# Performance work log

Hardware: AMD Instinct MI355X
Metric: run time of the kernel (lower is better)

## Reference

```python
import jax, jax.numpy as jnp
import numpy as np

BN_EPS = 1e-5
SG = jax.lax.stop_gradient


def _silu(z):
    return z * jax.nn.sigmoid(z)


def _binary_activation(x):
    # forward value = sign(x); backward goes through piecewise quadratic out3 (STE)
    out1 = jnp.where(x < -1, -1.0, x * x + 2 * x)
    out2 = jnp.where(x < 0, out1, -x * x + 2 * x)
    out3 = jnp.where(x < 1, out2, 1.0)
    return SG(jnp.sign(x)) - SG(out3) + out3


def _binarize_weight(w):
    # per-output-channel scaling factor * sign(w), STE through clipped weights
    sf = SG(jnp.mean(jnp.abs(w), axis=(1, 2, 3), keepdims=True))  # [O,1,1,1]
    cw = jnp.clip(w, -1.0, 1.0)
    return SG(sf * jnp.sign(w)) - SG(cw) + cw


def _conv3x3_s2(x, w, b):
    y = jax.lax.conv_general_dilated(
        x, w, window_strides=(2, 2), padding=((1, 1), (1, 1)),
        dimension_numbers=("NCHW", "OIHW", "NCHW"))
    return y + b[None, :, None, None]


def _batchnorm_train(x, gamma, beta):
    # training-mode BN: batch statistics over (N,H,W), biased variance
    mean = jnp.mean(x, axis=(0, 2, 3), keepdims=True)
    var = jnp.mean((x - mean) ** 2, axis=(0, 2, 3), keepdims=True)
    xhat = (x - mean) * jax.lax.rsqrt(var + BN_EPS)
    return xhat * gamma[None, :, None, None] + beta[None, :, None, None]


def _learnable_bias(x, emb, w, b):
    # bias = zero_module(linear)(SiLU(emb)) broadcast over H,W
    bias = _silu(emb) @ w.T + b  # [B, C]
    return x + bias[:, :, None, None]


def _avgpool2(x):
    B, C, H, W = x.shape
    return x.reshape(B, C, H // 2, 2, W // 2, 2).mean(axis=(3, 5))


def setup_inputs() -> dict:
    key = jax.random.key(0)
    ks = jax.random.split(key, 16)
    B, Cin, P, E, H, W = 32, 128, 256, 512, 64, 64
    scalor = P // Cin  # 2
    inp = {
        "x": jax.random.normal(ks[0], (B, Cin, H, W), jnp.float32),
        "emb": jax.random.normal(ks[1], (B, E), jnp.float32),
        "m1_w": jax.random.normal(ks[2], (Cin, E), jnp.float32) * 0.02,
        "m1_b": jnp.zeros((Cin,), jnp.float32),
        "conv_w": jax.random.uniform(ks[3], (scalor, Cin, Cin, 3, 3), jnp.float32, -1.0, 1.0) * 0.1,
        "conv_b": jax.random.normal(ks[4], (scalor, Cin), jnp.float32) * 0.01,
        "bn_g": jnp.ones((scalor, Cin), jnp.float32),
        "bn_b": jnp.zeros((scalor, Cin), jnp.float32),
        "m2_w": jax.random.normal(ks[5], (P, E), jnp.float32) * 0.02,
        "m2_b": jnp.zeros((P,), jnp.float32),
        "prelu_a": jnp.full((P,), 0.25, jnp.float32),
        "m3_w": jax.random.normal(ks[6], (P, E), jnp.float32) * 0.02,
        "m3_b": jnp.zeros((P,), jnp.float32),
    }
    return inp


def reference(x, emb, m1_w, m1_b, conv_w, conv_b, bn_g, bn_b,
              m2_w, m2_b, prelu_a, m3_w, m3_b):
    scalor = conv_w.shape[0]
    out = _learnable_bias(x, emb, m1_w, m1_b)
    out = _binary_activation(out)
    xp = _avgpool2(x)  # residual, [B,Cin,H/2,W/2]
    out_list = []
    for i in range(scalor):
        bw = _binarize_weight(conv_w[i])
        y = _conv3x3_s2(out, bw, conv_b[i])
        y = _batchnorm_train(y, bn_g[i], bn_b[i])
        out_list.append(y + xp)
    o = jnp.concatenate(out_list, axis=1)  # [B, planes, H/2, W/2]
    o = _learnable_bias(o, emb, m2_w, m2_b)
    a = prelu_a[None, :, None, None]
    o = jnp.where(o > 0, o, a * o)  # PReLU per channel
    o = _learnable_bias(o, emb, m3_w, m3_b)
    return o
```

## Files before the change

### kernel.cpp

```cpp
#include <hip/hip_runtime.h>
#include <cstdint>
#include <cstddef>

#define B_  32
#define CIN 128
#define P_  256
#define E_  512
#define H_  64
#define W_  64
#define HO  32
#define WO  32

__global__ void k_bw(const float* __restrict__ emb,
                     const float* __restrict__ m1_w, const float* __restrict__ m1_b,
                     const float* __restrict__ m2_w, const float* __restrict__ m2_b,
                     const float* __restrict__ m3_w, const float* __restrict__ m3_b,
                     const float* __restrict__ conv_w,
                     float* __restrict__ b1, float* __restrict__ b2, float* __restrict__ b3,
                     float* __restrict__ sf, unsigned int* __restrict__ wbits,
                     float* __restrict__ s1, float* __restrict__ s2) {
    int bid = blockIdx.x;
    int tid = threadIdx.x;
    int wave = tid >> 6, lane = tid & 63;

    if (bid < B_ * 160) {
        int n = bid / 160, rg = bid % 160;
        int row = rg * 4 + wave;
        const float* sp = emb + n * E_;
        const float* wrow; float bias; float* dst;
        if (row < CIN)            { wrow = m1_w + (size_t)row * E_;          bias = m1_b[row]; dst = b1 + n * CIN + row; }
        else if (row < CIN + P_)  { int c = row - CIN;      wrow = m2_w + (size_t)c * E_; bias = m2_b[c]; dst = b2 + n * P_ + c; }
        else                      { int c = row - CIN - P_; wrow = m3_w + (size_t)c * E_; bias = m3_b[c]; dst = b3 + n * P_ + c; }
        float acc = 0.f;
        #pragma unroll
        for (int j = 0; j < 8; j++) {
            int k = j * 64 + lane;
            float e = sp[k];
            acc += (e / (1.f + expf(-e))) * wrow[k];
        }
        #pragma unroll
        for (int off = 32; off > 0; off >>= 1) acc += __shfl_down(acc, off);
        if (lane == 0) *dst = acc + bias;
        return;
    }

    int base = (bid - B_ * 160) * 2;
    int oc = base + (wave >> 1);
    int iw = wave & 1;
    int i  = iw * 64 + lane;
    if (lane == 0 && iw == 0) { s1[oc] = 0.f; s2[oc] = 0.f; }
    const float* wp = conv_w + ((size_t)oc * CIN + i) * 9;
    float w[9]; float s = 0.f;
    #pragma unroll
    for (int t = 0; t < 9; t++) { w[t] = wp[t]; s += fabsf(w[t]); }
    #pragma unroll
    for (int t = 0; t < 9; t++) {
        unsigned long long m = __ballot(w[t] < 0.f);
        if (lane == 0) {
            wbits[oc * 36 + t * 4 + iw * 2 + 0] = (unsigned int)(m & 0xffffffffull);
            wbits[oc * 36 + t * 4 + iw * 2 + 1] = (unsigned int)(m >> 32);
        }
    }
    #pragma unroll
    for (int off = 32; off > 0; off >>= 1) s += __shfl_down(s, off);
    __shared__ float sred[4];
    if (lane == 0) sred[wave] = s;
    __syncthreads();
    if (tid == 0)        sf[base]     = (sred[0] + sred[1]) / 1152.f;
    else if (tid == 128) sf[base + 1] = (sred[2] + sred[3]) / 1152.f;
}

__global__ void k_prep(const float* __restrict__ x, const float* __restrict__ b1,
                       unsigned int* __restrict__ abits, float* __restrict__ xpool) {
    __shared__ float sb1[CIN];
    int n = blockIdx.x >> 5, h2 = blockIdx.x & 31;
    int tid = threadIdx.x;
    for (int i = tid; i < CIN; i += 256) sb1[i] = b1[n * CIN + i];
    __syncthreads();

    int pix = tid >> 1, half = tid & 1;
    int h = 2 * h2 + (pix >> 6), w = pix & 63;
    const float* xp = x + ((size_t)n * CIN + half * 64) * (H_ * W_) + (size_t)h * W_ + w;
    unsigned int wds[2];
    #pragma unroll
    for (int wd = 0; wd < 2; wd++) {
        unsigned int m = 0;
        #pragma unroll
        for (int b = 0; b < 32; b++) {
            float v = xp[(size_t)(wd * 32 + b) * (H_ * W_)] + sb1[half * 64 + wd * 32 + b];
            m |= (v < 0.f ? 1u : 0u) << b;
        }
        wds[wd] = m;
    }
    ((uint2*)abits)[((size_t)n * 4096 + (size_t)h * 64 + w) * 2 + half] = make_uint2(wds[0], wds[1]);

    for (int idx = tid; idx < CIN * WO; idx += 256) {
        int c = idx >> 5, w2 = idx & 31;
        const float* p = x + ((size_t)n * CIN + c) * (H_ * W_) + (size_t)(2 * h2) * W_ + 2 * w2;
        float2 a = *(const float2*)p;
        float2 b = *(const float2*)(p + W_);
        xpool[((size_t)n * CIN + c) * (HO * WO) + h2 * WO + w2] = 0.25f * (a.x + a.y + b.x + b.y);
    }
}

__global__ void __launch_bounds__(256, 4) k_conv(const unsigned int* __restrict__ abits,
                                                 const unsigned int* __restrict__ wbits,
                                                 const float* __restrict__ sf,
                                                 float* __restrict__ y) {
    int bid = blockIdx.x;
    int strip = bid & 3, ocg = (bid >> 2) & 7, n = bid >> 5;
    int tid = threadIdx.x;
    int oh = strip * 8 + (tid >> 5), ow = tid & 31;

    const uint4* asrc = ((const uint4*)abits) + ((size_t)n << 12);
    uint4 img[9]; int vmask = 0;
    #pragma unroll
    for (int kh = 0; kh < 3; kh++) {
        #pragma unroll
        for (int kw = 0; kw < 3; kw++) {
            int t = kh * 3 + kw;
            int r = 2 * oh - 1 + kh, c = 2 * ow - 1 + kw;
            bool v = (unsigned)r < 64u && (unsigned)c < 64u;
            img[t] = v ? asrc[r * 64 + c] : make_uint4(0u, 0u, 0u, 0u);
            vmask |= (v ? 1 : 0) << t;
        }
    }
    int base128 = 128 * __popc(vmask);

    const uint4* wp = ((const uint4*)wbits) + (size_t)ocg * 32 * 9;
    const float* sfp = sf + ocg * 32;
    float* yp = y + (((size_t)n * P_ + ocg * 32) << 10) + strip * 256 + tid;
    #pragma unroll 4
    for (int o = 0; o < 32; o++) {
        int popsum = 0;
        #pragma unroll
        for (int t = 0; t < 9; t++) {
            uint4 a = img[t];
            uint4 w = wp[o * 9 + t];
            int p = __popc(a.x ^ w.x) + __popc(a.y ^ w.y) +
                    __popc(a.z ^ w.z) + __popc(a.w ^ w.w);
            popsum += ((vmask >> t) & 1) ? p : 0;
        }
        yp[(size_t)o << 10] = sfp[o] * (float)(base128 - 2 * popsum);
    }
}

__global__ void k_stats(const float* __restrict__ y,
                        float* __restrict__ s1, float* __restrict__ s2) {
    int c = blockIdx.x >> 2, q = blockIdx.x & 3;
    int tid = threadIdx.x;
    float s = 0.f, ss = 0.f;
    for (int n = q * 8; n < q * 8 + 8; n++) {
        float4 v = ((const float4*)y)[(((size_t)n * P_ + c) << 8) + tid];
        s  += v.x + v.y + v.z + v.w;
        ss += v.x * v.x + v.y * v.y + v.z * v.z + v.w * v.w;
    }
    #pragma unroll
    for (int off = 32; off > 0; off >>= 1) {
        s += __shfl_down(s, off); ss += __shfl_down(ss, off);
    }
    __shared__ float r1[4], r2[4];
    int wave = tid >> 6, lane = tid & 63;
    if (lane == 0) { r1[wave] = s; r2[wave] = ss; }
    __syncthreads();
    if (tid == 0) {
        atomicAdd(s1 + c, r1[0] + r1[1] + r1[2] + r1[3]);
        atomicAdd(s2 + c, r2[0] + r2[1] + r2[2] + r2[3]);
    }
}

__global__ void k_epi(float* __restrict__ y, const float* __restrict__ xpool,
                      const float* __restrict__ s1, const float* __restrict__ s2,
                      const float* __restrict__ bn_g, const float* __restrict__ bn_b,
                      const float* __restrict__ b2, const float* __restrict__ b3,
                      const float* __restrict__ prelu_a) {
    int i4 = blockIdx.x * blockDim.x + threadIdx.x;
    int pix4 = i4 & 255;
    int c = (i4 >> 8) & 255;
    int n = i4 >> 16;
    float4 yv = ((const float4*)y)[i4];
    float4 xv = ((const float4*)xpool)[((n * CIN + (c & 127)) << 8) + pix4];
    const float inv = 1.f / (B_ * HO * WO);
    float m = s1[c] * inv;
    float var = fmaf(-m, m, s2[c] * inv);
    float r = rsqrtf(var + 1e-5f) * bn_g[c];
    float add0 = bn_b[c] + b2[n * P_ + c];
    float a = prelu_a[c];
    float b3v = b3[n * P_ + c];
    float o0 = (yv.x - m) * r + add0 + xv.x; o0 = (o0 > 0.f ? o0 : a * o0) + b3v;
    float o1 = (yv.y - m) * r + add0 + xv.y; o1 = (o1 > 0.f ? o1 : a * o1) + b3v;
    float o2 = (yv.z - m) * r + add0 + xv.z; o2 = (o2 > 0.f ? o2 : a * o2) + b3v;
    float o3 = (yv.w - m) * r + add0 + xv.w; o3 = (o3 > 0.f ? o3 : a * o3) + b3v;
    ((float4*)y)[i4] = make_float4(o0, o1, o2, o3);
}

extern "C" void kernel_launch(void* const* d_in, const int* in_sizes, int n_in,
                              void* d_out, int out_size, void* d_ws, size_t ws_size,
                              hipStream_t stream) {
    const float* x      = (const float*)d_in[0];
    const float* emb    = (const float*)d_in[1];
    const float* m1_w   = (const float*)d_in[2];
    const float* m1_b   = (const float*)d_in[3];
    const float* conv_w = (const float*)d_in[4];
    const float* bn_g   = (const float*)d_in[6];
    const float* bn_b   = (const float*)d_in[7];
    const float* m2_w   = (const float*)d_in[8];
    const float* m2_b   = (const float*)d_in[9];
    const float* prelu_a= (const float*)d_in[10];
    const float* m3_w   = (const float*)d_in[11];
    const float* m3_b   = (const float*)d_in[12];

    float* y = (float*)d_out;

    float* wsf = (float*)d_ws;
    float* b1    = wsf;
    float* b2    = wsf + 4096;
    float* b3    = wsf + 12288;
    float* sf    = wsf + 20480;
    float* s1    = wsf + 20736;
    float* s2    = wsf + 20992;
    unsigned int* wbits = (unsigned int*)(wsf + 21248);
    unsigned int* abits = (unsigned int*)(wsf + 30464);
    float* xpool = wsf + 554752;

    k_bw   <<<B_ * 160 + P_ / 2, 256, 0, stream>>>(emb, m1_w, m1_b, m2_w, m2_b, m3_w, m3_b,
                                                   conv_w, b1, b2, b3, sf, wbits, s1, s2);
    k_prep <<<B_ * 32, 256, 0, stream>>>(x, b1, abits, xpool);
    k_conv <<<B_ * 32, 256, 0, stream>>>(abits, wbits, sf, y);
    k_stats<<<P_ * 4, 256, 0, stream>>>(y, s1, s2);
    k_epi  <<<(B_ * P_ * HO * WO) / (4 * 256), 256, 0, stream>>>(y, xpool, s1, s2,
                                                                 bn_g, bn_b, b2, b3, prelu_a);
}
```

Baseline: 195.2 us.

## Fuse BN statistics into binary conv and store conv output as int16

The binary convolution now writes its raw integer popcount result as int16 to a workspace buffer, and reduces per-channel sum and sum of squares in-kernel through shuffles, shared memory and atomics. This removes the separate stats kernel and its full re-read of the fp32 conv output, and halves the size of the intermediate tensor. The per-channel scale factor is applied in the epilogue, which also recomputes mean and variance from the integer sums. The cost is extra shuffle and shared-memory work plus a block barrier inside the conv kernel.

```diff
diff --git a/kernel.cpp b/kernel.cpp
--- a/kernel.cpp
+++ b/kernel.cpp
@@ -103,13 +103,15 @@
     }
 }
 
-__global__ void __launch_bounds__(256, 4) k_conv(const unsigned int* __restrict__ abits,
-                                                 const unsigned int* __restrict__ wbits,
-                                                 const float* __restrict__ sf,
-                                                 float* __restrict__ y) {
+__global__ void __launch_bounds__(256, 4) k_convstat(const unsigned int* __restrict__ abits,
+                                                     const unsigned int* __restrict__ wbits,
+                                                     short* __restrict__ y16,
+                                                     float* __restrict__ s1, float* __restrict__ s2) {
+    __shared__ int red1[32][33], red2[32][33];
     int bid = blockIdx.x;
     int strip = bid & 3, ocg = (bid >> 2) & 7, n = bid >> 5;
     int tid = threadIdx.x;
+    int wave = tid >> 6, lane = tid & 63;
     int oh = strip * 8 + (tid >> 5), ow = tid & 31;
 
     const uint4* asrc = ((const uint4*)abits) + ((size_t)n << 12);
@@ -128,8 +130,7 @@
     int base128 = 128 * __popc(vmask);
 
     const uint4* wp = ((const uint4*)wbits) + (size_t)ocg * 32 * 9;
-    const float* sfp = sf + ocg * 32;
-    float* yp = y + (((size_t)n * P_ + ocg * 32) << 10) + strip * 256 + tid;
+    short* yp = y16 + (((size_t)n * P_ + ocg * 32) << 10) + strip * 256 + tid;
     #pragma unroll 4
     for (int o = 0; o < 32; o++) {
         int popsum = 0;
@@ -141,57 +142,55 @@
                     __popc(a.z ^ w.z) + __popc(a.w ^ w.w);
             popsum += ((vmask >> t) & 1) ? p : 0;
         }
-        yp[(size_t)o << 10] = sfp[o] * (float)(base128 - 2 * popsum);
-    }
-}
-
-__global__ void k_stats(const float* __restrict__ y,
-                        float* __restrict__ s1, float* __restrict__ s2) {
-    int c = blockIdx.x >> 2, q = blockIdx.x & 3;
-    int tid = threadIdx.x;
-    float s = 0.f, ss = 0.f;
-    for (int n = q * 8; n < q * 8 + 8; n++) {
-        float4 v = ((const float4*)y)[(((size_t)n * P_ + c) << 8) + tid];
-        s  += v.x + v.y + v.z + v.w;
-        ss += v.x * v.x + v.y * v.y + v.z * v.z + v.w * v.w;
-    }
-    #pragma unroll
-    for (int off = 32; off > 0; off >>= 1) {
-        s += __shfl_down(s, off); ss += __shfl_down(ss, off);
-    }
-    __shared__ float r1[4], r2[4];
-    int wave = tid >> 6, lane = tid & 63;
-    if (lane == 0) { r1[wave] = s; r2[wave] = ss; }
+        int s = base128 - 2 * popsum;
+        yp[(size_t)o << 10] = (short)s;
+        int vs = s, v2 = s * s;
+        vs += __shfl_down(vs, 32); v2 += __shfl_down(v2, 32);
+        vs += __shfl_down(vs, 16); v2 += __shfl_down(v2, 16);
+        vs += __shfl_down(vs, 8);  v2 += __shfl_down(v2, 8);
+        if (lane < 8) { red1[o][wave * 8 + lane] = vs; red2[o][wave * 8 + lane] = v2; }
+    }
     __syncthreads();
-    if (tid == 0) {
-        atomicAdd(s1 + c, r1[0] + r1[1] + r1[2] + r1[3]);
-        atomicAdd(s2 + c, r2[0] + r2[1] + r2[2] + r2[3]);
-    }
-}
-
-__global__ void k_epi(float* __restrict__ y, const float* __restrict__ xpool,
+    if (tid < 64) {
+        int o = tid & 31;
+        int a = 0;
+        if (tid < 32) {
+            #pragma unroll
+            for (int p = 0; p < 32; p++) a += red1[o][p];
+            atomicAdd(s1 + ocg * 32 + o, (float)a);
+        } else {
+            #pragma unroll
+            for (int p = 0; p < 32; p++) a += red2[o][p];
+            atomicAdd(s2 + ocg * 32 + o, (float)a);
+        }
+    }
+}
+
+__global__ void k_epi(const short* __restrict__ y16, const float* __restrict__ xpool,
+                      const float* __restrict__ sf,
                       const float* __restrict__ s1, const float* __restrict__ s2,
                       const float* __restrict__ bn_g, const float* __restrict__ bn_b,
                       const float* __restrict__ b2, const float* __restrict__ b3,
-                      const float* __restrict__ prelu_a) {
+                      const float* __restrict__ prelu_a, float* __restrict__ out) {
     int i4 = blockIdx.x * blockDim.x + threadIdx.x;
     int pix4 = i4 & 255;
     int c = (i4 >> 8) & 255;
     int n = i4 >> 16;
-    float4 yv = ((const float4*)y)[i4];
+    short4 yv = ((const short4*)y16)[i4];
     float4 xv = ((const float4*)xpool)[((n * CIN + (c & 127)) << 8) + pix4];
     const float inv = 1.f / (B_ * HO * WO);
-    float m = s1[c] * inv;
-    float var = fmaf(-m, m, s2[c] * inv);
+    float sc = sf[c];
+    float m = sc * s1[c] * inv;
+    float var = fmaf(-m, m, sc * sc * s2[c] * inv);
     float r = rsqrtf(var + 1e-5f) * bn_g[c];
     float add0 = bn_b[c] + b2[n * P_ + c];
     float a = prelu_a[c];
     float b3v = b3[n * P_ + c];
-    float o0 = (yv.x - m) * r + add0 + xv.x; o0 = (o0 > 0.f ? o0 : a * o0) + b3v;
-    float o1 = (yv.y - m) * r + add0 + xv.y; o1 = (o1 > 0.f ? o1 : a * o1) + b3v;
-    float o2 = (yv.z - m) * r + add0 + xv.z; o2 = (o2 > 0.f ? o2 : a * o2) + b3v;
-    float o3 = (yv.w - m) * r + add0 + xv.w; o3 = (o3 > 0.f ? o3 : a * o3) + b3v;
-    ((float4*)y)[i4] = make_float4(o0, o1, o2, o3);
+    float o0 = (sc * (float)yv.x - m) * r + add0 + xv.x; o0 = (o0 > 0.f ? o0 : a * o0) + b3v;
+    float o1 = (sc * (float)yv.y - m) * r + add0 + xv.y; o1 = (o1 > 0.f ? o1 : a * o1) + b3v;
+    float o2 = (sc * (float)yv.z - m) * r + add0 + xv.z; o2 = (o2 > 0.f ? o2 : a * o2) + b3v;
+    float o3 = (sc * (float)yv.w - m) * r + add0 + xv.w; o3 = (o3 > 0.f ? o3 : a * o3) + b3v;
+    ((float4*)out)[i4] = make_float4(o0, o1, o2, o3);
 }
 
 extern "C" void kernel_launch(void* const* d_in, const int* in_sizes, int n_in,
@@ -210,7 +209,7 @@
     const float* m3_w   = (const float*)d_in[11];
     const float* m3_b   = (const float*)d_in[12];
 
-    float* y = (float*)d_out;
+    float* out = (float*)d_out;
 
     float* wsf = (float*)d_ws;
     float* b1    = wsf;
@@ -222,12 +221,12 @@
     unsigned int* wbits = (unsigned int*)(wsf + 21248);
     unsigned int* abits = (unsigned int*)(wsf + 30464);
     float* xpool = wsf + 554752;
-
-    k_bw   <<<B_ * 160 + P_ / 2, 256, 0, stream>>>(emb, m1_w, m1_b, m2_w, m2_b, m3_w, m3_b,
-                                                   conv_w, b1, b2, b3, sf, wbits, s1, s2);
-    k_prep <<<B_ * 32, 256, 0, stream>>>(x, b1, abits, xpool);
-    k_conv <<<B_ * 32, 256, 0, stream>>>(abits, wbits, sf, y);
-    k_stats<<<P_ * 4, 256, 0, stream>>>(y, s1, s2);
-    k_epi  <<<(B_ * P_ * HO * WO) / (4 * 256), 256, 0, stream>>>(y, xpool, s1, s2,
-                                                                 bn_g, bn_b, b2, b3, prelu_a);
-}
+    short* y16   = (short*)(wsf + 4749056 + 16384);
+
+    k_bw      <<<B_ * 160 + P_ / 2, 256, 0, stream>>>(emb, m1_w, m1_b, m2_w, m2_b, m3_w, m3_b,
+                                                      conv_w, b1, b2, b3, sf, wbits, s1, s2);
+    k_prep    <<<B_ * 32, 256, 0, stream>>>(x, b1, abits, xpool);
+    k_convstat<<<B_ * 32, 256, 0, stream>>>(abits, wbits, y16, s1, s2);
+    k_epi     <<<(B_ * P_ * HO * WO) / (4 * 256), 256, 0, stream>>>(y16, xpool, sf, s1, s2,
+                                                                    bn_g, bn_b, b2, b3, prelu_a, out);
+}
```

After: 190.4 us. -2.5%, faster.
